# Optimization experiments

Hardware: AMD Instinct MI355X
Metric: run time of the kernel (lower is better)

The kernel has to match this reference:

```python
import jax, jax.numpy as jnp
import numpy as np
from jax import lax

B, L, D_MODEL = 4, 1024, 512
D_STATE, D_CONV, D_INNER = 16, 4, 2 * D_MODEL


def setup_inputs() -> dict:
    key = jax.random.key(0)
    ks = jax.random.split(key, 8)
    s = 0.02
    x = jax.random.normal(ks[0], (B, L, D_MODEL), dtype=jnp.float32)
    W_in = jax.random.normal(ks[1], (D_MODEL, 2 * D_INNER), dtype=jnp.float32) * s
    conv_w = jax.random.normal(ks[2], (D_INNER, 1, D_CONV), dtype=jnp.float32) * s  # OIH, depthwise
    conv_b = jnp.zeros((D_INNER,), jnp.float32)
    W_x = jax.random.normal(ks[3], (D_INNER, 2 * D_STATE), dtype=jnp.float32) * s
    W_dt = jax.random.normal(ks[4], (D_INNER, D_INNER), dtype=jnp.float32) * s
    b_dt = jnp.zeros((D_INNER,), jnp.float32)
    # A_log = -logspace(log10(0.001), log10(1.0), d_state); used directly as A in the scan
    A_log = -jnp.logspace(np.log10(1e-3), 0.0, D_STATE, dtype=jnp.float32)
    D_skip = jnp.ones((D_INNER,), jnp.float32) * 0.1
    W_out = jax.random.normal(ks[5], (D_INNER, D_MODEL), dtype=jnp.float32) * s
    gamma = jnp.ones((D_MODEL,), jnp.float32)
    beta = jnp.zeros((D_MODEL,), jnp.float32)
    return dict(x=x, W_in=W_in, conv_w=conv_w, conv_b=conv_b, W_x=W_x, W_dt=W_dt,
                b_dt=b_dt, A_log=A_log, D_skip=D_skip, W_out=W_out, gamma=gamma, beta=beta)


def _mamba_forward(x, W_in, conv_w, conv_b, W_x, W_dt, b_dt, A_log, D_skip, W_out, gamma, beta):
    x = jnp.clip(x, -10.0, 10.0)
    x_and_res = x @ W_in                                  # [B, L, 2*d_inner]
    xp, res = jnp.split(x_and_res, 2, axis=-1)
    # Depthwise causal conv1d: torch pads d_conv-1 both sides then slices [:L] -> left-pad only.
    xt = jnp.transpose(xp, (0, 2, 1))                     # [B, d_inner, L]
    xc = lax.conv_general_dilated(xt, conv_w, window_strides=(1,),
                                  padding=[(D_CONV - 1, 0)],
                                  dimension_numbers=('NCH', 'OIH', 'NCH'),
                                  feature_group_count=D_INNER)
    xc = xc + conv_b[None, :, None]
    xc = jax.nn.silu(jnp.transpose(xc, (0, 2, 1)))        # [B, L, d_inner]
    ssm = xc @ W_x                                        # [B, L, 2*d_state]
    Bm, Cm = jnp.split(ssm, 2, axis=-1)                   # each [B, L, d_state]
    delta = xc @ W_dt + b_dt                              # [B, L, d_inner] (no softplus in source)

    # Selective scan over time (sequential recurrence)
    def step(h, inp):
        u_t, d_t, B_t, C_t = inp                          # [B,I], [B,I], [B,S], [B,S]
        dA = jnp.exp(jnp.clip(d_t[:, :, None] * A_log, -5.0, 5.0))   # [B, I, S]
        h = dA * h + (d_t[:, :, None] * B_t[:, None, :]) * u_t[:, :, None]
        y = jnp.einsum('bis,bs->bi', h, C_t)
        return h, y

    tm = lambda a: jnp.swapaxes(a, 0, 1)                  # time-major
    h0 = jnp.zeros((x.shape[0], D_INNER, D_STATE), xc.dtype)
    _, ys = lax.scan(step, h0, (tm(xc), tm(delta), tm(Bm), tm(Cm)))
    y = jnp.swapaxes(ys, 0, 1) + xc * D_skip              # D skip connection

    y = y * jax.nn.silu(res)                              # gating
    out = y @ W_out
    r = out + x                                           # residual
    mu = jnp.mean(r, axis=-1, keepdims=True)
    var = jnp.var(r, axis=-1, keepdims=True)
    return gamma * (r - mu) / jnp.sqrt(var + 1e-5) + beta


def reference(x, W_in, conv_w, conv_b, W_x, W_dt, b_dt, A_log, D_skip, W_out, gamma, beta):
    return _mamba_forward(x, W_in, conv_w, conv_b, W_x, W_dt, b_dt, A_log, D_skip, W_out, gamma, beta)
```

## Files before the change

### kernel.cpp

```cpp
#include <hip/hip_runtime.h>
#include <hip/hip_bf16.h>

typedef __hip_bfloat16 bf16;
typedef unsigned short ushort_t;
typedef unsigned int uint_t;
typedef __attribute__((ext_vector_type(8))) __bf16 bf16x8;
typedef __attribute__((ext_vector_type(8))) ushort_t u16x8;
typedef __attribute__((ext_vector_type(4))) ushort_t u16x4;
typedef __attribute__((ext_vector_type(4))) float f32x4;

#define BB 4
#define LL 1024
#define DM 512
#define DS 16
#define DI 1024
#define ROWS 4096
#define NC 128
#define CT 8
#define NCH 8
#define NDTX 1152

__device__ __forceinline__ float b2f(bf16 v) { return __bfloat162float(v); }

__device__ __forceinline__ float load_flag(const void* src, int i, int isbf)
{
    return isbf ? b2f(((const bf16*)src)[i]) : ((const float*)src)[i];
}

__device__ __forceinline__ ushort_t f2b_bits(float v)
{
    bf16 t = __float2bfloat16(v);
    return *(ushort_t*)&t;
}

__device__ __forceinline__ float bits2f(ushort_t u)
{
    uint_t w = ((uint_t)u) << 16;
    return __uint_as_float(w);
}

__device__ __forceinline__ int detect_local(const ushort_t* wdt)
{
    __shared__ int bad;
    if (threadIdx.x == 0) bad = 0;
    __syncthreads();
    ushort_t u = wdt[threadIdx.x & 255];
    if (((u >> 7) & 0xFF) >= 127) atomicAdd(&bad, 1);
    __syncthreads();
    return (bad <= 8) ? 1 : 0;
}

__global__ __launch_bounds__(256)
void prep_all(const void* x, const void* Win, const void* Wdt, const void* Wx,
              const void* Wout, const void* cw, const void* cb, const void* Alog,
              const void* Dsk, const void* gam, const void* bet, const void* bdtin,
              bf16* __restrict__ xbf, bf16* __restrict__ WtIn,
              bf16* __restrict__ WtDtx, bf16* __restrict__ WtOut,
              float* __restrict__ ccw, float* __restrict__ ccb,
              float* __restrict__ cAlg, float* __restrict__ cDsk,
              float* __restrict__ cgam, float* __restrict__ cbet,
              float* __restrict__ bdtx)
{
    const int isbf = detect_local((const ushort_t*)Wdt);
    int blk = blockIdx.x;

    if (blk < 2048) {
        int idx = blk * 256 + threadIdx.x;
        float v[4];
        if (isbf) {
            uint2 raw = ((const uint2*)x)[idx];
            v[0] = __uint_as_float(raw.x << 16);
            v[1] = __uint_as_float(raw.x & 0xFFFF0000u);
            v[2] = __uint_as_float(raw.y << 16);
            v[3] = __uint_as_float(raw.y & 0xFFFF0000u);
        } else {
            float4 raw = ((const float4*)x)[idx];
            v[0] = raw.x; v[1] = raw.y; v[2] = raw.z; v[3] = raw.w;
        }
        uint_t b0, b1;
        b0 = f2b_bits(fminf(fmaxf(v[0], -10.f), 10.f))
           | ((uint_t)f2b_bits(fminf(fmaxf(v[1], -10.f), 10.f)) << 16);
        b1 = f2b_bits(fminf(fmaxf(v[2], -10.f), 10.f))
           | ((uint_t)f2b_bits(fminf(fmaxf(v[3], -10.f), 10.f)) << 16);
        uint2 ow; ow.x = b0; ow.y = b1;
        ((uint2*)xbf)[idx] = ow;
    } else if (blk < 4640) {
        int tb = blk - 2048;
        const void* src; bf16* dst; int K, Nsrc, tpr;
        if (tb < 1024)      { src = Win;  dst = WtIn;   K = 512;  Nsrc = 2048; tpr = 64; }
        else if (tb < 2048) { tb -= 1024; src = Wdt;  dst = WtDtx; K = 1024; Nsrc = 1024; tpr = 32; }
        else if (tb < 2080) { tb -= 2048; src = Wx;   dst = WtDtx + 1024 * 1024; K = 1024; Nsrc = 32; tpr = 1; }
        else                { tb -= 2080; src = Wout; dst = WtOut;  K = 1024; Nsrc = 512;  tpr = 16; }
        int k0 = (tb / tpr) * 32, n0 = (tb % tpr) * 32;

        __shared__ float tile[32][33];
        int tx = threadIdx.x & 31, ty = threadIdx.x >> 5;
        #pragma unroll
        for (int j = 0; j < 4; ++j)
            tile[ty + 8 * j][tx] = load_flag(src, (k0 + ty + 8 * j) * Nsrc + n0 + tx, isbf);
        __syncthreads();
        #pragma unroll
        for (int j = 0; j < 4; ++j)
            dst[(size_t)(n0 + ty + 8 * j) * K + k0 + tx] = __float2bfloat16(tile[tx][ty + 8 * j]);
    } else {
        int i = (blk - 4640) * 256 + threadIdx.x;
        if (i < 4096)        ccw[i] = load_flag(cw, i, isbf);
        else if (i < 5120)   ccb[i - 4096] = load_flag(cb, i - 4096, isbf);
        else if (i < 5136)   cAlg[i - 5120] = load_flag(Alog, i - 5120, isbf);
        else if (i < 6160)   cDsk[i - 5136] = load_flag(Dsk, i - 5136, isbf);
        else if (i < 6672)   cgam[i - 6160] = load_flag(gam, i - 6160, isbf);
        else if (i < 7184)   cbet[i - 6672] = load_flag(bet, i - 6672, isbf);
        else if (i < 8336) {
            int j = i - 7184;
            bdtx[j] = (j < DI) ? load_flag(bdtin, j, isbf) : 0.f;
        } else if (i < 106640) {
            (WtDtx + 1056 * 1024)[i - 8336] = __float2bfloat16(0.f);
        }
    }
}

__device__ __forceinline__ void gload16(const bf16* g, ushort_t* l)
{
    __builtin_amdgcn_global_load_lds(
        (const __attribute__((address_space(1))) void*)g,
        (__attribute__((address_space(3))) void*)l, 16, 0, 0);
}

template <int TM, int TN, bool OBF, bool OT, bool SPLIT>
__global__ __launch_bounds__(256)
void gemm_mfma(const bf16* __restrict__ A, const bf16* __restrict__ Bt,
               const float* __restrict__ bias, void* __restrict__ Cv,
               void* __restrict__ Cv2, int M, int N, int K)
{
    constexpr int MI = TM / 32, NJ = TN / 32;
    constexpr int NQA = TM * 8 / 256;
    constexpr int NQB = TN * 8 / 256;
    __shared__ ushort_t As[TM * 64];
    __shared__ ushort_t Bs[TN * 64];

    const int tid = threadIdx.x;
    const int lane = tid & 63;
    const int w = tid >> 6;
    const int wr = w >> 1, wc = w & 1;
    const int m0 = blockIdx.y * TM;
    const int n0 = blockIdx.x * TN;

    const bf16* gA[NQA]; ushort_t* lA[NQA];
    #pragma unroll
    for (int q = 0; q < NQA; ++q) {
        int p = q * 256 + tid;
        int row = p >> 3, kc = ((p & 7) - row) & 7;
        gA[q] = A + (size_t)(m0 + row) * K + kc * 8;
        lA[q] = &As[(q * 256 + w * 64) * 8];
    }
    const bf16* gB[NQB]; ushort_t* lB[NQB];
    #pragma unroll
    for (int q = 0; q < NQB; ++q) {
        int p = q * 256 + tid;
        int row = p >> 3, kc = ((p & 7) - row) & 7;
        gB[q] = Bt + (size_t)(n0 + row) * K + kc * 8;
        lB[q] = &Bs[(q * 256 + w * 64) * 8];
    }

    f32x4 acc[MI][NJ];
    #pragma unroll
    for (int i = 0; i < MI; ++i)
        #pragma unroll
        for (int j = 0; j < NJ; ++j)
            acc[i][j] = (f32x4){0.f, 0.f, 0.f, 0.f};

    const int ko = lane >> 4;
    const int ml = lane & 15;

    for (int k0 = 0; k0 < K; k0 += 64) {
        #pragma unroll
        for (int q = 0; q < NQA; ++q) gload16(gA[q] + k0, lA[q]);
        #pragma unroll
        for (int q = 0; q < NQB; ++q) gload16(gB[q] + k0, lB[q]);
        __syncthreads();

        #pragma unroll
        for (int half = 0; half < 2; ++half) {
            bf16x8 af[MI], bfr[NJ];
            #pragma unroll
            for (int i = 0; i < MI; ++i) {
                int m = wr * (TM / 2) + i * 16 + ml;
                af[i] = *(const bf16x8*)&As[(m * 8 + ((half * 4 + ko + m) & 7)) * 8];
            }
            #pragma unroll
            for (int j = 0; j < NJ; ++j) {
                int n = wc * (TN / 2) + j * 16 + ml;
                bfr[j] = *(const bf16x8*)&Bs[(n * 8 + ((half * 4 + ko + n) & 7)) * 8];
            }
            #pragma unroll
            for (int i = 0; i < MI; ++i)
                #pragma unroll
                for (int j = 0; j < NJ; ++j)
                    acc[i][j] = __builtin_amdgcn_mfma_f32_16x16x32_bf16(
                        af[i], bfr[j], acc[i][j], 0, 0, 0);
        }
        __syncthreads();
    }

    const int rq = lane >> 4;
    #pragma unroll
    for (int j = 0; j < NJ; ++j) {
        int n = n0 + wc * (TN / 2) + j * 16 + ml;
        float bv = bias ? bias[n] : 0.f;
        #pragma unroll
        for (int i = 0; i < MI; ++i) {
            int mb = m0 + wr * (TM / 2) + i * 16 + rq * 4;
            if (SPLIT && n >= 1024) {
                if (n < 1088) {
                    #pragma unroll
                    for (int r = 0; r < 4; ++r)
                        ((bf16*)Cv2)[(size_t)(mb + r) * 64 + (n - 1024)] =
                            __float2bfloat16(acc[i][j][r] + bv);
                }
            } else if (OT) {
                u16x4 pk;
                #pragma unroll
                for (int r = 0; r < 4; ++r)
                    pk[r] = f2b_bits(acc[i][j][r] + bv);
                *(u16x4*)((ushort_t*)Cv + (size_t)n * M + mb) = pk;
            } else {
                #pragma unroll
                for (int r = 0; r < 4; ++r) {
                    float v = acc[i][j][r] + bv;
                    if (OBF) ((bf16*)Cv)[(size_t)(mb + r) * N + n] = __float2bfloat16(v);
                    else     ((float*)Cv)[(size_t)(mb + r) * N + n] = v;
                }
            }
        }
    }
}

__global__ __launch_bounds__(256)
void conv_silu(const bf16* __restrict__ xrbT, const float* __restrict__ cw,
               const float* __restrict__ cb, bf16* __restrict__ xcT,
               bf16* __restrict__ xc)
{
    __shared__ ushort_t tile[64 * 72];
    const int blk = blockIdx.x;
    const int ch0 = (blk & 15) * 64;
    const int T0b = (blk >> 4) * 64;
    const int lc = threadIdx.x >> 2, tg = threadIdx.x & 3;
    const int i = ch0 + lc;
    const int T0 = T0b + tg * 16;

    const ushort_t* base = (const ushort_t*)xrbT + (size_t)i * ROWS + T0;
    u16x8 m0 = *(const u16x8*)base;
    u16x8 m1 = *(const u16x8*)(base + 8);
    u16x8 pv = {0, 0, 0, 0, 0, 0, 0, 0};
    if ((T0 & (LL - 1)) != 0) pv = *(const u16x8*)(base - 8);

    float4 w = ((const float4*)cw)[i];
    float bs = cb[i];
    float xm3 = bits2f(pv[5]), xm2 = bits2f(pv[6]), xm1 = bits2f(pv[7]);
    u16x8 o0, o1;
    #pragma unroll
    for (int tt = 0; tt < 16; ++tt) {
        float x0 = bits2f(tt < 8 ? m0[tt] : m1[tt - 8]);
        float acc = bs;
        acc = fmaf(xm3, w.x, acc);
        acc = fmaf(xm2, w.y, acc);
        acc = fmaf(xm1, w.z, acc);
        acc = fmaf(x0,  w.w, acc);
        ushort_t ob = f2b_bits(acc / (1.f + __expf(-acc)));
        if (tt < 8) o0[tt] = ob; else o1[tt - 8] = ob;
        xm3 = xm2; xm2 = xm1; xm1 = x0;
    }
    ushort_t* dt = (ushort_t*)xcT + (size_t)i * ROWS + T0;
    *(u16x8*)dt = o0;
    *(u16x8*)(dt + 8) = o1;
    *(u16x8*)&tile[lc * 72 + tg * 16] = o0;
    *(u16x8*)&tile[lc * 72 + tg * 16 + 8] = o1;
    __syncthreads();
    const int lt = threadIdx.x >> 2, cg = threadIdx.x & 3;
    u16x8 q0, q1;
    #pragma unroll
    for (int j = 0; j < 8; ++j) q0[j] = tile[(cg * 16 + j) * 72 + lt];
    #pragma unroll
    for (int j = 8; j < 16; ++j) q1[j - 8] = tile[(cg * 16 + j) * 72 + lt];
    ushort_t* wp = (ushort_t*)xc + (size_t)(T0b + lt) * DI + ch0 + cg * 16;
    *(u16x8*)wp = q0;
    *(u16x8*)(wp + 8) = q1;
}

__global__ __launch_bounds__(1024)
void scan_fused(const bf16* __restrict__ xcT, const bf16* __restrict__ dT,
                const bf16* __restrict__ ssm, const bf16* __restrict__ xrbT,
                const float* __restrict__ A_log, const float* __restrict__ Dskip,
                bf16* __restrict__ ybf)
{
    __shared__ uint_t lsum[DS * NC * NCH];

    const int tid = threadIdx.x;
    const int b = blockIdx.x >> 7;
    const int ch0 = (blockIdx.x & 127) << 3;
    const int chl = tid & 7;
    const int c = tid >> 3;
    const int i = ch0 + chl;
    const size_t tb = (size_t)b * LL + c * CT;

    float a[DS];
    #pragma unroll
    for (int s = 0; s < DS; ++s) {
        uint_t bits = (uint_t)__builtin_amdgcn_readfirstlane((int)__float_as_uint(A_log[s]));
        a[s] = __uint_as_float(bits);
    }

    const u16x8* dp = (const u16x8*)((const ushort_t*)dT + (size_t)i * ROWS + tb);
    const u16x8* up = (const u16x8*)((const ushort_t*)xcT + (size_t)i * ROWS + tb);
    const u16x8* rp = (const u16x8*)((const ushort_t*)xrbT + (size_t)(1024 + i) * ROWS + tb);

    float h[DS] = {};
    float p[DS];
    #pragma unroll
    for (int s = 0; s < DS; ++s) p[s] = 1.f;

    {
        u16x8 dv8 = dp[0];
        u16x8 uv8 = up[0];
        #pragma unroll
        for (int t = 0; t < CT; ++t) {
            float dv = bits2f(dv8[t]);
            float uv = bits2f(uv8[t]);
            float du = dv * uv;
            const u16x8* sp = (const u16x8*)((const ushort_t*)ssm + (tb + t) * 64);
            u16x8 B0 = sp[0], B1 = sp[1];
            #pragma unroll
            for (int s = 0; s < DS; ++s) {
                float e = fminf(fmaxf(dv * a[s], -5.f), 5.f);
                float dA = __expf(e);
                float Bv = bits2f(s < 8 ? B0[s] : B1[s - 8]);
                h[s] = fmaf(dA, h[s], du * Bv);
                p[s] *= dA;
            }
        }
    }
    #pragma unroll
    for (int s = 0; s < DS; ++s)
        lsum[s * (NC * NCH) + tid] = (uint_t)f2b_bits(p[s]) | ((uint_t)f2b_bits(h[s]) << 16);
    __syncthreads();

    if (tid < NCH * DS) {
        int cl = tid & 7, s = tid >> 3;
        float hh = 0.f;
        for (int cc = 0; cc < NC; ++cc) {
            int off = s * (NC * NCH) + cc * NCH + cl;
            uint_t wrd = lsum[off];
            float pp = bits2f((ushort_t)(wrd & 0xFFFF));
            float qq = bits2f((ushort_t)(wrd >> 16));
            lsum[off] = (uint_t)f2b_bits(hh);
            hh = fmaf(pp, hh, qq);
        }
    }
    __syncthreads();

    #pragma unroll
    for (int s = 0; s < DS; ++s) h[s] = bits2f((ushort_t)lsum[s * (NC * NCH) + tid]);

    const float dsk = Dskip[i];

    {
        u16x8 dv8 = dp[0];
        u16x8 uv8 = up[0];
        u16x8 rv8 = rp[0];
        #pragma unroll
        for (int t = 0; t < CT; ++t) {
            float dv = bits2f(dv8[t]);
            float uv = bits2f(uv8[t]);
            float du = dv * uv;
            const u16x8* sp = (const u16x8*)((const ushort_t*)ssm + (tb + t) * 64);
            u16x8 B0 = sp[0], B1 = sp[1], C0 = sp[2], C1 = sp[3];
            float y = 0.f;
            #pragma unroll
            for (int s = 0; s < DS; ++s) {
                float e = fminf(fmaxf(dv * a[s], -5.f), 5.f);
                float dA = __expf(e);
                float Bv = bits2f(s < 8 ? B0[s] : B1[s - 8]);
                float Cc = bits2f(s < 8 ? C0[s] : C1[s - 8]);
                h[s] = fmaf(dA, h[s], du * Bv);
                y = fmaf(h[s], Cc, y);
            }
            float res = bits2f(rv8[t]);
            float g = res / (1.f + __expf(-res));
            ybf[(tb + t) * DI + i] = __float2bfloat16((y + uv * dsk) * g);
        }
    }
}

__global__ __launch_bounds__(256)
void ln_kernel(const bf16* __restrict__ outp, const void* __restrict__ xsrc,
               const void* __restrict__ wdt_probe,
               const float* __restrict__ gamma, const float* __restrict__ beta,
               void* __restrict__ out)
{
    const int isbf = detect_local((const ushort_t*)wdt_probe);
    const int row = blockIdx.x;
    const int tid = threadIdx.x;

    float r[2];
    float sum = 0.f, ss = 0.f;
    #pragma unroll
    for (int q = 0; q < 2; ++q) {
        int j = tid + q * 256;
        float xv = load_flag(xsrc, row * DM + j, isbf);
        xv = fminf(fmaxf(xv, -10.f), 10.f);
        float v = b2f(outp[(size_t)row * DM + j]) + xv;
        r[q] = v;
        sum += v;
        ss = fmaf(v, v, ss);
    }
    #pragma unroll
    for (int off = 32; off >= 1; off >>= 1) {
        sum += __shfl_down(sum, off);
        ss  += __shfl_down(ss, off);
    }
    __shared__ float s1[4], s2[4];
    __shared__ float stats[2];
    int wid = tid >> 6, lane = tid & 63;
    if (lane == 0) { s1[wid] = sum; s2[wid] = ss; }
    __syncthreads();
    if (tid == 0) {
        float S = s1[0] + s1[1] + s1[2] + s1[3];
        float Qq = s2[0] + s2[1] + s2[2] + s2[3];
        float mean = S / DM;
        float var = Qq / DM - mean * mean;
        stats[0] = mean;
        stats[1] = rsqrtf(var + 1e-5f);
    }
    __syncthreads();
    float mean = stats[0], rstd = stats[1];
    #pragma unroll
    for (int q = 0; q < 2; ++q) {
        int j = tid + q * 256;
        float v = (r[q] - mean) * rstd * gamma[j] + beta[j];
        size_t o = (size_t)row * DM + j;
        if (isbf) ((bf16*)out)[o] = __float2bfloat16(v);
        else      ((float*)out)[o] = v;
    }
}

extern "C" void kernel_launch(void* const* d_in, const int* in_sizes, int n_in,
                              void* d_out, int out_size, void* d_ws, size_t ws_size,
                              hipStream_t stream)
{
    float* W = (float*)d_ws;
    float* ccw  = W;
    float* ccb  = ccw  + 4096;
    float* cAlg = ccb  + 1024;
    float* cDsk = cAlg + 16;
    float* cgam = cDsk + 1024;
    float* cbet = cgam + 512;
    float* bdtx = cbet + 512;
    bf16*  xbf  = (bf16*)(bdtx + 1152);
    bf16*  xrbT = xbf  + 2097152;
    bf16*  xcT  = xrbT + 8388608;
    bf16*  xc   = xcT  + 4194304;
    bf16*  ybf  = xc   + 4194304;
    bf16*  dT   = ybf  + 4194304;
    bf16*  ssm  = dT   + 4194304;
    bf16*  outp = ssm  + 262144;
    bf16*  WtIn = outp + 2097152;
    bf16*  WtDtx= WtIn + 1048576;
    bf16*  WtOut= WtDtx+ 1179648;

    prep_all<<<5057, 256, 0, stream>>>(
        d_in[0], d_in[1], d_in[5], d_in[4], d_in[9], d_in[2], d_in[3],
        d_in[7], d_in[8], d_in[10], d_in[11], d_in[6],
        xbf, WtIn, WtDtx, WtOut, ccw, ccb, cAlg, cDsk, cgam, cbet, bdtx);

    gemm_mfma<64, 128, true, true, false><<<dim3(2048 / 128, ROWS / 64), 256, 0, stream>>>(
        xbf, WtIn, nullptr, xrbT, nullptr, ROWS, 2048, 512);

    conv_silu<<<1024, 256, 0, stream>>>(xrbT, ccw, ccb, xcT, xc);

    gemm_mfma<64, 128, true, true, true><<<dim3(NDTX / 128, ROWS / 64), 256, 0, stream>>>(
        xc, WtDtx, bdtx, dT, ssm, ROWS, NDTX, DI);

    scan_fused<<<512, 1024, 0, stream>>>(xcT, dT, ssm, xrbT, cAlg, cDsk, ybf);

    gemm_mfma<64, 64, true, false, false><<<dim3(DM / 64, ROWS / 64), 256, 0, stream>>>(
        ybf, WtOut, nullptr, outp, nullptr, ROWS, DM, DI);

    ln_kernel<<<ROWS, 256, 0, stream>>>(outp, d_in[0], d_in[5], cgam, cbet, d_out);
}
```

Measured before the change: 219.7 us.

## Restructure scan chunking, store B/C in fp32, use exp2, enlarge in-proj GEMM tile

The selective scan now uses 64 chunks of 16 timesteps with 16 channels per block and launches 256 blocks instead of 512. The B/C projections are stored as fp32 and read as float4 vectors. The exponent is pre-scaled by log2(e) so exp2f can be used with rescaled clip bounds. The input-projection GEMM tile grows to 128x128. The aim is less per-element unpacking and serial carry work, traded against lower scan occupancy and more B/C memory traffic.

```diff
diff --git a/kernel.cpp b/kernel.cpp
--- a/kernel.cpp
+++ b/kernel.cpp
@@ -15,10 +15,11 @@
 #define DS 16
 #define DI 1024
 #define ROWS 4096
-#define NC 128
-#define CT 8
-#define NCH 8
+#define NC 64
+#define CT 16
 #define NDTX 1152
+
+#define CLP2 7.21347520f
 
 __device__ __forceinline__ float b2f(bf16 v) { return __bfloat162float(v); }
 
@@ -214,8 +215,8 @@
                 if (n < 1088) {
                     #pragma unroll
                     for (int r = 0; r < 4; ++r)
-                        ((bf16*)Cv2)[(size_t)(mb + r) * 64 + (n - 1024)] =
-                            __float2bfloat16(acc[i][j][r] + bv);
+                        ((float*)Cv2)[(size_t)(mb + r) * 64 + (n - 1024)] =
+                            acc[i][j][r] + bv;
                 }
             } else if (OT) {
                 u16x4 pk;
@@ -289,25 +290,25 @@
 
 __global__ __launch_bounds__(1024)
 void scan_fused(const bf16* __restrict__ xcT, const bf16* __restrict__ dT,
-                const bf16* __restrict__ ssm, const bf16* __restrict__ xrbT,
+                const float* __restrict__ ssm, const bf16* __restrict__ xrbT,
                 const float* __restrict__ A_log, const float* __restrict__ Dskip,
                 bf16* __restrict__ ybf)
 {
-    __shared__ uint_t lsum[DS * NC * NCH];
+    __shared__ uint_t lsum[DS * NC * 16];
 
     const int tid = threadIdx.x;
-    const int b = blockIdx.x >> 7;
-    const int ch0 = (blockIdx.x & 127) << 3;
-    const int chl = tid & 7;
-    const int c = tid >> 3;
+    const int b = blockIdx.x >> 6;
+    const int ch0 = (blockIdx.x & 63) << 4;
+    const int chl = tid & 15;
+    const int c = tid >> 4;
     const int i = ch0 + chl;
     const size_t tb = (size_t)b * LL + c * CT;
 
-    float a[DS];
+    float a2[DS];
     #pragma unroll
     for (int s = 0; s < DS; ++s) {
         uint_t bits = (uint_t)__builtin_amdgcn_readfirstlane((int)__float_as_uint(A_log[s]));
-        a[s] = __uint_as_float(bits);
+        a2[s] = __uint_as_float(bits) * 1.44269504f;
     }
 
     const u16x8* dp = (const u16x8*)((const ushort_t*)dT + (size_t)i * ROWS + tb);
@@ -319,36 +320,40 @@
     #pragma unroll
     for (int s = 0; s < DS; ++s) p[s] = 1.f;
 
-    {
-        u16x8 dv8 = dp[0];
-        u16x8 uv8 = up[0];
-        #pragma unroll
-        for (int t = 0; t < CT; ++t) {
+    #pragma unroll
+    for (int half = 0; half < 2; ++half) {
+        u16x8 dv8 = dp[half];
+        u16x8 uv8 = up[half];
+        #pragma unroll
+        for (int t = 0; t < 8; ++t) {
             float dv = bits2f(dv8[t]);
             float uv = bits2f(uv8[t]);
             float du = dv * uv;
-            const u16x8* sp = (const u16x8*)((const ushort_t*)ssm + (tb + t) * 64);
-            u16x8 B0 = sp[0], B1 = sp[1];
+            const f32x4* sv = (const f32x4*)(ssm + (tb + half * 8 + t) * 64);
             #pragma unroll
-            for (int s = 0; s < DS; ++s) {
-                float e = fminf(fmaxf(dv * a[s], -5.f), 5.f);
-                float dA = __expf(e);
-                float Bv = bits2f(s < 8 ? B0[s] : B1[s - 8]);
-                h[s] = fmaf(dA, h[s], du * Bv);
-                p[s] *= dA;
+            for (int g = 0; g < 4; ++g) {
+                f32x4 Bq = sv[g];
+                #pragma unroll
+                for (int q = 0; q < 4; ++q) {
+                    int s = g * 4 + q;
+                    float e = fminf(fmaxf(dv * a2[s], -CLP2), CLP2);
+                    float dA = exp2f(e);
+                    h[s] = fmaf(dA, h[s], du * Bq[q]);
+                    p[s] *= dA;
+                }
             }
         }
     }
     #pragma unroll
     for (int s = 0; s < DS; ++s)
-        lsum[s * (NC * NCH) + tid] = (uint_t)f2b_bits(p[s]) | ((uint_t)f2b_bits(h[s]) << 16);
-    __syncthreads();
-
-    if (tid < NCH * DS) {
-        int cl = tid & 7, s = tid >> 3;
+        lsum[s * 1024 + tid] = (uint_t)f2b_bits(p[s]) | ((uint_t)f2b_bits(h[s]) << 16);
+    __syncthreads();
+
+    if (tid < 256) {
+        int cl = tid & 15, s = tid >> 4;
         float hh = 0.f;
         for (int cc = 0; cc < NC; ++cc) {
-            int off = s * (NC * NCH) + cc * NCH + cl;
+            int off = s * 1024 + cc * 16 + cl;
             uint_t wrd = lsum[off];
             float pp = bits2f((ushort_t)(wrd & 0xFFFF));
             float qq = bits2f((ushort_t)(wrd >> 16));
@@ -359,34 +364,38 @@
     __syncthreads();
 
     #pragma unroll
-    for (int s = 0; s < DS; ++s) h[s] = bits2f((ushort_t)lsum[s * (NC * NCH) + tid]);
+    for (int s = 0; s < DS; ++s) h[s] = bits2f((ushort_t)lsum[s * 1024 + tid]);
 
     const float dsk = Dskip[i];
 
-    {
-        u16x8 dv8 = dp[0];
-        u16x8 uv8 = up[0];
-        u16x8 rv8 = rp[0];
-        #pragma unroll
-        for (int t = 0; t < CT; ++t) {
+    #pragma unroll
+    for (int half = 0; half < 2; ++half) {
+        u16x8 dv8 = dp[half];
+        u16x8 uv8 = up[half];
+        u16x8 rv8 = rp[half];
+        #pragma unroll
+        for (int t = 0; t < 8; ++t) {
             float dv = bits2f(dv8[t]);
             float uv = bits2f(uv8[t]);
             float du = dv * uv;
-            const u16x8* sp = (const u16x8*)((const ushort_t*)ssm + (tb + t) * 64);
-            u16x8 B0 = sp[0], B1 = sp[1], C0 = sp[2], C1 = sp[3];
+            const f32x4* sv = (const f32x4*)(ssm + (tb + half * 8 + t) * 64);
             float y = 0.f;
             #pragma unroll
-            for (int s = 0; s < DS; ++s) {
-                float e = fminf(fmaxf(dv * a[s], -5.f), 5.f);
-                float dA = __expf(e);
-                float Bv = bits2f(s < 8 ? B0[s] : B1[s - 8]);
-                float Cc = bits2f(s < 8 ? C0[s] : C1[s - 8]);
-                h[s] = fmaf(dA, h[s], du * Bv);
-                y = fmaf(h[s], Cc, y);
+            for (int g = 0; g < 4; ++g) {
+                f32x4 Bq = sv[g];
+                f32x4 Cq = sv[4 + g];
+                #pragma unroll
+                for (int q = 0; q < 4; ++q) {
+                    int s = g * 4 + q;
+                    float e = fminf(fmaxf(dv * a2[s], -CLP2), CLP2);
+                    float dA = exp2f(e);
+                    h[s] = fmaf(dA, h[s], du * Bq[q]);
+                    y = fmaf(h[s], Cq[q], y);
+                }
             }
             float res = bits2f(rv8[t]);
-            float g = res / (1.f + __expf(-res));
-            ybf[(tb + t) * DI + i] = __float2bfloat16((y + uv * dsk) * g);
+            float g2 = res / (1.f + __expf(-res));
+            ybf[(tb + half * 8 + t) * DI + i] = __float2bfloat16((y + uv * dsk) * g2);
         }
     }
 }
@@ -455,14 +464,14 @@
     float* cgam = cDsk + 1024;
     float* cbet = cgam + 512;
     float* bdtx = cbet + 512;
-    bf16*  xbf  = (bf16*)(bdtx + 1152);
+    float* ssm  = bdtx + 1152;
+    bf16*  xbf  = (bf16*)(ssm + 262144);
     bf16*  xrbT = xbf  + 2097152;
     bf16*  xcT  = xrbT + 8388608;
     bf16*  xc   = xcT  + 4194304;
     bf16*  ybf  = xc   + 4194304;
     bf16*  dT   = ybf  + 4194304;
-    bf16*  ssm  = dT   + 4194304;
-    bf16*  outp = ssm  + 262144;
+    bf16*  outp = dT   + 4194304;
     bf16*  WtIn = outp + 2097152;
     bf16*  WtDtx= WtIn + 1048576;
     bf16*  WtOut= WtDtx+ 1179648;
@@ -472,7 +481,7 @@
         d_in[7], d_in[8], d_in[10], d_in[11], d_in[6],
         xbf, WtIn, WtDtx, WtOut, ccw, ccb, cAlg, cDsk, cgam, cbet, bdtx);
 
-    gemm_mfma<64, 128, true, true, false><<<dim3(2048 / 128, ROWS / 64), 256, 0, stream>>>(
+    gemm_mfma<128, 128, true, true, false><<<dim3(2048 / 128, ROWS / 128), 256, 0, stream>>>(
         xbf, WtIn, nullptr, xrbT, nullptr, ROWS, 2048, 512);
 
     conv_silu<<<1024, 256, 0, stream>>>(xrbT, ccw, ccb, xcT, xc);
@@ -480,7 +489,7 @@
     gemm_mfma<64, 128, true, true, true><<<dim3(NDTX / 128, ROWS / 64), 256, 0, stream>>>(
         xc, WtDtx, bdtx, dT, ssm, ROWS, NDTX, DI);
 
-    scan_fused<<<512, 1024, 0, stream>>>(xcT, dT, ssm, xrbT, cAlg, cDsk, ybf);
+    scan_fused<<<256, 1024, 0, stream>>>(xcT, dT, ssm, xrbT, cAlg, cDsk, ybf);
 
     gemm_mfma<64, 64, true, false, false><<<dim3(DM / 64, ROWS / 64), 256, 0, stream>>>(
         ybf, WtOut, nullptr, outp, nullptr, ROWS, DM, DI);
```

New measurement: 219.2 us. Within noise of the previous version (-0.2%).
